# Kernel optimization log

Measured on AMD Instinct MI355X. Metric: run time of the kernel, lower is better.

Reference implementation:

```python
import jax, jax.numpy as jnp
import numpy as np

N_NODES = 50000
N_EDGES = 800000
D_FEAT = 128


def setup_inputs() -> dict:
    key = jax.random.key(0)
    k1, k2, k3, k4 = jax.random.split(key, 4)
    x = jax.random.normal(k1, (N_NODES, D_FEAT), dtype=jnp.float32)
    vals = jax.random.uniform(k2, (N_EDGES,), dtype=jnp.float32)
    rows = jnp.sort(jax.random.randint(k3, (N_EDGES,), 0, N_NODES, dtype=jnp.int32))
    cols = jax.random.randint(k4, (N_EDGES,), 0, N_NODES, dtype=jnp.int32)
    return {"x": x, "vals": vals, "rows": rows, "cols": cols}


def reference(x, vals, rows, cols):
    # out = A @ x where A is sparse COO: out[r] += vals[e] * x[cols[e]] for each edge e with rows[e]==r
    messages = vals[:, None] * x[cols]  # [E, d]
    out = jax.ops.segment_sum(messages, rows, num_segments=N_NODES)  # [N, d]
    return out
```

## Files before the change

kernel.cpp:

```cpp
#include <hip/hip_runtime.h>


#define D_FEAT 128
#define TOTAL_WAVES 8192
#define WAVES_PER_BLOCK 4
#define BLOCK_THREADS (WAVES_PER_BLOCK * 64)
#define PF 8

typedef float v2f __attribute__((ext_vector_type(2)));

__device__ __forceinline__ float bcast_f(float v, int j) {
    return __int_as_float(__builtin_amdgcn_readlane(__float_as_int(v), j));
}

__device__ __forceinline__ unsigned short f2bf_rne(float f) {
    unsigned int b = __float_as_uint(f);
    b += 0x7fffu + ((b >> 16) & 1u);
    return (unsigned short)(b >> 16);
}

__global__ __launch_bounds__(256) void prep_kernel(
    const float* __restrict__ x, const int* __restrict__ rows,
    unsigned short* __restrict__ xb, int* __restrict__ row_ptr,
    float* __restrict__ out, int n4, int n_edges, int n_nodes) {
    const int tid = blockIdx.x * blockDim.x + threadIdx.x;
    const int nth = gridDim.x * blockDim.x;
    const float4* __restrict__ x4 = (const float4*)x;
    ushort4* __restrict__ o4 = (ushort4*)xb;
    for (int i = tid; i < n4; i += nth) {
        float4 f = x4[i];
        ushort4 o;
        o.x = f2bf_rne(f.x);
        o.y = f2bf_rne(f.y);
        o.z = f2bf_rne(f.z);
        o.w = f2bf_rne(f.w);
        o4[i] = o;
    }
    for (int e = tid; e <= n_edges; e += nth) {
        int r, rp;
        if (e < n_edges) {
            r  = rows[e];
            rp = (e == 0) ? -1 : rows[e - 1];
        } else {
            r  = n_nodes;
            rp = rows[n_edges - 1];
        }
        for (int q = rp + 1; q <= r; ++q)
            if (q <= n_nodes) row_ptr[q] = e;
        for (int q = rp + 1; q < r && q < n_nodes; ++q) {
            float4* zo = (float4*)(out + (size_t)q * D_FEAT);
            for (int k = 0; k < D_FEAT / 4; ++k) zo[k] = make_float4(0.f, 0.f, 0.f, 0.f);
        }
    }
}

__global__ __launch_bounds__(BLOCK_THREADS) void agg_bf16_kernel(
    const unsigned int* __restrict__ xb,
    const float* __restrict__ vals, const int* __restrict__ rows,
    const int* __restrict__ cols, const int* __restrict__ row_ptr,
    float* __restrict__ out, int n_edges, int n_nodes, int epw) {
    const int wave = blockIdx.x * WAVES_PER_BLOCK + (threadIdx.x >> 6);
    const int lane = threadIdx.x & 63;

    const int s = wave * epw;
    if (s >= n_edges) return;
    const int s2 = min(s + epw, n_edges);

    int lo = 0, hi = n_nodes;
    while (lo < hi) {
        int mid = (lo + hi) >> 1;
        if (row_ptr[mid] < s) lo = mid + 1; else hi = mid;
    }
    const int r_lo = lo;
    hi = n_nodes;
    while (lo < hi) {
        int mid = (lo + hi) >> 1;
        if (row_ptr[mid] < s2) lo = mid + 1; else hi = mid;
    }
    const int start = row_ptr[r_lo];
    const int end   = row_ptr[lo];
    if (start >= end) return;

    int cur_row = rows[start];
    float2 acc = make_float2(0.f, 0.f);

    for (int e0 = start; e0 < end; e0 += 64) {
        const int nb = min(end - e0, 64);
        int myc = 0, myr = 0;
        float myv = 0.f;
        if (lane < nb) {
            myc = __builtin_nontemporal_load(cols + e0 + lane);
            myr = __builtin_nontemporal_load(rows + e0 + lane);
            myv = __builtin_nontemporal_load(vals + e0 + lane);
        }
        for (int j0 = 0; j0 < nb; j0 += PF) {
            const int m = min(nb - j0, PF);
            unsigned int xu[PF];
            int   rj[PF];
            float vj[PF];
#pragma unroll
            for (int t = 0; t < PF; ++t) {
                if (t < m) {
                    const int cj = __builtin_amdgcn_readlane(myc, j0 + t);
                    rj[t] = __builtin_amdgcn_readlane(myr, j0 + t);
                    vj[t] = bcast_f(myv, j0 + t);
                    xu[t] = xb[(size_t)cj * (D_FEAT / 2) + lane];
                }
            }
#pragma unroll
            for (int t = 0; t < PF; ++t) {
                if (t < m) {
                    if (rj[t] != cur_row) {
                        v2f st; st.x = acc.x; st.y = acc.y;
                        __builtin_nontemporal_store(
                            st, (v2f*)(out + (size_t)cur_row * D_FEAT + 2 * lane));
                        acc.x = 0.f; acc.y = 0.f;
                        cur_row = rj[t];
                    }
                    const float x0 = __uint_as_float(xu[t] << 16);
                    const float x1 = __uint_as_float(xu[t] & 0xffff0000u);
                    acc.x = fmaf(vj[t], x0, acc.x);
                    acc.y = fmaf(vj[t], x1, acc.y);
                }
            }
        }
    }
    v2f st; st.x = acc.x; st.y = acc.y;
    __builtin_nontemporal_store(st, (v2f*)(out + (size_t)cur_row * D_FEAT + 2 * lane));
}

__global__ __launch_bounds__(BLOCK_THREADS) void agg_f32_kernel(
    const float* __restrict__ x, const float* __restrict__ vals,
    const int* __restrict__ rows, const int* __restrict__ cols,
    float* __restrict__ out, int n_edges, int epw) {
    const int wave = blockIdx.x * WAVES_PER_BLOCK + (threadIdx.x >> 6);
    const int lane = threadIdx.x & 63;

    const int start = wave * epw;
    if (start >= n_edges) return;
    int end = start + epw;
    if (end > n_edges) end = n_edges;

    const float2* __restrict__ x2 = (const float2*)x;
    const int first_row = rows[start];
    const int last_row  = rows[end - 1];

    float2 acc = make_float2(0.f, 0.f);
    int cur_row = first_row;

    for (int e0 = start; e0 < end; e0 += 64) {
        const int nb = min(end - e0, 64);
        int myc = 0, myr = 0;
        float myv = 0.f;
        if (lane < nb) {
            myc = cols[e0 + lane];
            myr = rows[e0 + lane];
            myv = vals[e0 + lane];
        }
        for (int j0 = 0; j0 < nb; j0 += PF) {
            const int m = min(nb - j0, PF);
            float2 xv[PF];
            int    rj[PF];
            float  vj[PF];
#pragma unroll
            for (int t = 0; t < PF; ++t) {
                if (t < m) {
                    const int cj = __builtin_amdgcn_readlane(myc, j0 + t);
                    rj[t] = __builtin_amdgcn_readlane(myr, j0 + t);
                    vj[t] = bcast_f(myv, j0 + t);
                    xv[t] = x2[(size_t)cj * (D_FEAT / 2) + lane];
                }
            }
#pragma unroll
            for (int t = 0; t < PF; ++t) {
                if (t < m) {
                    if (rj[t] != cur_row) {
                        float* o = out + (size_t)cur_row * D_FEAT + 2 * lane;
                        if (cur_row == first_row || cur_row == last_row) {
                            atomicAdd(o,     acc.x);
                            atomicAdd(o + 1, acc.y);
                        } else {
                            v2f st; st.x = acc.x; st.y = acc.y;
                            __builtin_nontemporal_store(st, (v2f*)o);
                        }
                        acc.x = 0.f; acc.y = 0.f;
                        cur_row = rj[t];
                    }
                    acc.x = fmaf(vj[t], xv[t].x, acc.x);
                    acc.y = fmaf(vj[t], xv[t].y, acc.y);
                }
            }
        }
    }
    float* o = out + (size_t)cur_row * D_FEAT + 2 * lane;
    atomicAdd(o,     acc.x);
    atomicAdd(o + 1, acc.y);
}

extern "C" void kernel_launch(void* const* d_in, const int* in_sizes, int n_in,
                              void* d_out, int out_size, void* d_ws, size_t ws_size,
                              hipStream_t stream) {
    const float* x    = (const float*)d_in[0];
    const float* vals = (const float*)d_in[1];
    const int*   rows = (const int*)d_in[2];
    const int*   cols = (const int*)d_in[3];
    float*       out  = (float*)d_out;

    const int n_edges = in_sizes[1];
    const int n_x     = in_sizes[0];
    const int n_nodes = out_size / D_FEAT;

    const int epw    = (n_edges + TOTAL_WAVES - 1) / TOTAL_WAVES;
    const int blocks = TOTAL_WAVES / WAVES_PER_BLOCK;

    const size_t xb_bytes = (size_t)n_x * sizeof(unsigned short);
    const size_t rp_off   = (xb_bytes + 255) & ~(size_t)255;
    const size_t need     = rp_off + (size_t)(n_nodes + 1) * sizeof(int);

    if (ws_size >= need) {
        unsigned short* xb = (unsigned short*)d_ws;
        int* row_ptr = (int*)((char*)d_ws + rp_off);
        prep_kernel<<<2048, 256, 0, stream>>>(x, rows, xb, row_ptr, out,
                                              n_x / 4, n_edges, n_nodes);
        agg_bf16_kernel<<<blocks, BLOCK_THREADS, 0, stream>>>(
            (const unsigned int*)xb, vals, rows, cols, row_ptr, out,
            n_edges, n_nodes, epw);
    } else {
        (void)hipMemsetAsync(d_out, 0, (size_t)out_size * sizeof(float), stream);
        agg_f32_kernel<<<blocks, BLOCK_THREADS, 0, stream>>>(
            x, vals, rows, cols, out, n_edges, epw);
    }
}
```

Before: 131.2 us.

## Switch bf16 aggregation to dynamic row-chunk scheduling via atomic work counter

The bf16 aggregation kernel drops the static edge split with per-wave binary searches over row_ptr. Each wave now takes chunks of two rows from a global atomic counter, which prep_kernel resets to zero. Row boundaries come from row_ptr instead of reading the rows array. This removes the binary-search cost and balances load dynamically, at the price of one atomic per two rows (about 25k atomics on a single counter) and very small work items per grab.

```diff
diff --git a/kernel.cpp b/kernel.cpp
--- a/kernel.cpp
+++ b/kernel.cpp
@@ -4,8 +4,10 @@
 #define D_FEAT 128
 #define TOTAL_WAVES 8192
 #define WAVES_PER_BLOCK 4
-#define BLOCK_THREADS (WAVES_PER_BLOCK * 64)
+#define BLOCK_THREADS 256
+#define NBLOCKS (TOTAL_WAVES / WAVES_PER_BLOCK)
 #define PF 8
+#define RPC 2
 
 typedef float v2f __attribute__((ext_vector_type(2)));
 
@@ -22,9 +24,11 @@
 __global__ __launch_bounds__(256) void prep_kernel(
     const float* __restrict__ x, const int* __restrict__ rows,
     unsigned short* __restrict__ xb, int* __restrict__ row_ptr,
-    float* __restrict__ out, int n4, int n_edges, int n_nodes) {
+    int* __restrict__ ctr, float* __restrict__ out, int n4, int n_edges,
+    int n_nodes) {
     const int tid = blockIdx.x * blockDim.x + threadIdx.x;
     const int nth = gridDim.x * blockDim.x;
+    if (tid == 0) *ctr = 0;
     const float4* __restrict__ x4 = (const float4*)x;
     ushort4* __restrict__ o4 = (ushort4*)xb;
     for (int i = tid; i < n4; i += nth) {
@@ -49,84 +53,78 @@
             if (q <= n_nodes) row_ptr[q] = e;
         for (int q = rp + 1; q < r && q < n_nodes; ++q) {
             float4* zo = (float4*)(out + (size_t)q * D_FEAT);
-            for (int k = 0; k < D_FEAT / 4; ++k) zo[k] = make_float4(0.f, 0.f, 0.f, 0.f);
+            for (int k = 0; k < D_FEAT / 4; ++k)
+                zo[k] = make_float4(0.f, 0.f, 0.f, 0.f);
         }
     }
 }
 
 __global__ __launch_bounds__(BLOCK_THREADS) void agg_bf16_kernel(
     const unsigned int* __restrict__ xb,
-    const float* __restrict__ vals, const int* __restrict__ rows,
-    const int* __restrict__ cols, const int* __restrict__ row_ptr,
-    float* __restrict__ out, int n_edges, int n_nodes, int epw) {
-    const int wave = blockIdx.x * WAVES_PER_BLOCK + (threadIdx.x >> 6);
+    const float* __restrict__ vals, const int* __restrict__ cols,
+    const int* __restrict__ row_ptr, int* __restrict__ ctr,
+    float* __restrict__ out, int n_nodes) {
     const int lane = threadIdx.x & 63;
-
-    const int s = wave * epw;
-    if (s >= n_edges) return;
-    const int s2 = min(s + epw, n_edges);
-
-    int lo = 0, hi = n_nodes;
-    while (lo < hi) {
-        int mid = (lo + hi) >> 1;
-        if (row_ptr[mid] < s) lo = mid + 1; else hi = mid;
-    }
-    const int r_lo = lo;
-    hi = n_nodes;
-    while (lo < hi) {
-        int mid = (lo + hi) >> 1;
-        if (row_ptr[mid] < s2) lo = mid + 1; else hi = mid;
-    }
-    const int start = row_ptr[r_lo];
-    const int end   = row_ptr[lo];
-    if (start >= end) return;
-
-    int cur_row = rows[start];
-    float2 acc = make_float2(0.f, 0.f);
-
-    for (int e0 = start; e0 < end; e0 += 64) {
-        const int nb = min(end - e0, 64);
-        int myc = 0, myr = 0;
-        float myv = 0.f;
-        if (lane < nb) {
-            myc = __builtin_nontemporal_load(cols + e0 + lane);
-            myr = __builtin_nontemporal_load(rows + e0 + lane);
-            myv = __builtin_nontemporal_load(vals + e0 + lane);
-        }
-        for (int j0 = 0; j0 < nb; j0 += PF) {
-            const int m = min(nb - j0, PF);
-            unsigned int xu[PF];
-            int   rj[PF];
-            float vj[PF];
-#pragma unroll
-            for (int t = 0; t < PF; ++t) {
-                if (t < m) {
-                    const int cj = __builtin_amdgcn_readlane(myc, j0 + t);
-                    rj[t] = __builtin_amdgcn_readlane(myr, j0 + t);
-                    vj[t] = bcast_f(myv, j0 + t);
-                    xu[t] = xb[(size_t)cj * (D_FEAT / 2) + lane];
-                }
-            }
-#pragma unroll
-            for (int t = 0; t < PF; ++t) {
-                if (t < m) {
-                    if (rj[t] != cur_row) {
-                        v2f st; st.x = acc.x; st.y = acc.y;
-                        __builtin_nontemporal_store(
-                            st, (v2f*)(out + (size_t)cur_row * D_FEAT + 2 * lane));
-                        acc.x = 0.f; acc.y = 0.f;
-                        cur_row = rj[t];
+    for (;;) {
+        int c = 0;
+        if (lane == 0) c = atomicAdd(ctr, 1);
+        c = __shfl(c, 0);
+        const int r0 = c * RPC;
+        if (r0 >= n_nodes) return;
+        const int r1 = min(r0 + RPC, n_nodes);
+        const int e_beg = row_ptr[r0];
+        const int e_end = row_ptr[r1];
+        if (e_beg >= e_end) continue;
+
+        int r = r0;
+        int next_b = row_ptr[r0 + 1];
+        int idx = e_beg;
+        float2 acc = make_float2(0.f, 0.f);
+
+        for (int e0 = e_beg; e0 < e_end; e0 += 64) {
+            const int nb = min(e_end - e0, 64);
+            int myc = 0;
+            float myv = 0.f;
+            if (lane < nb) {
+                myc = __builtin_nontemporal_load(cols + e0 + lane);
+                myv = __builtin_nontemporal_load(vals + e0 + lane);
+            }
+            for (int j0 = 0; j0 < nb; j0 += PF) {
+                const int m = min(nb - j0, PF);
+                unsigned int xu[PF];
+                float vj[PF];
+#pragma unroll
+                for (int t = 0; t < PF; ++t) {
+                    if (t < m) {
+                        const int cj = __builtin_amdgcn_readlane(myc, j0 + t);
+                        vj[t] = bcast_f(myv, j0 + t);
+                        xu[t] = xb[(size_t)cj * (D_FEAT / 2) + lane];
                     }
-                    const float x0 = __uint_as_float(xu[t] << 16);
-                    const float x1 = __uint_as_float(xu[t] & 0xffff0000u);
-                    acc.x = fmaf(vj[t], x0, acc.x);
-                    acc.y = fmaf(vj[t], x1, acc.y);
-                }
-            }
-        }
-    }
-    v2f st; st.x = acc.x; st.y = acc.y;
-    __builtin_nontemporal_store(st, (v2f*)(out + (size_t)cur_row * D_FEAT + 2 * lane));
+                }
+#pragma unroll
+                for (int t = 0; t < PF; ++t) {
+                    if (t < m) {
+                        while (idx == next_b) {
+                            v2f st; st.x = acc.x; st.y = acc.y;
+                            __builtin_nontemporal_store(
+                                st, (v2f*)(out + (size_t)r * D_FEAT + 2 * lane));
+                            acc.x = 0.f; acc.y = 0.f;
+                            ++r;
+                            next_b = row_ptr[r + 1];
+                        }
+                        const float x0 = __uint_as_float(xu[t] << 16);
+                        const float x1 = __uint_as_float(xu[t] & 0xffff0000u);
+                        acc.x = fmaf(vj[t], x0, acc.x);
+                        acc.y = fmaf(vj[t], x1, acc.y);
+                        ++idx;
+                    }
+                }
+            }
+        }
+        v2f st; st.x = acc.x; st.y = acc.y;
+        __builtin_nontemporal_store(
+            st, (v2f*)(out + (size_t)r * D_FEAT + 2 * lane));
+    }
 }
 
 __global__ __launch_bounds__(BLOCK_THREADS) void agg_f32_kernel(
@@ -210,24 +208,23 @@
     const int n_x     = in_sizes[0];
     const int n_nodes = out_size / D_FEAT;
 
-    const int epw    = (n_edges + TOTAL_WAVES - 1) / TOTAL_WAVES;
-    const int blocks = TOTAL_WAVES / WAVES_PER_BLOCK;
-
     const size_t xb_bytes = (size_t)n_x * sizeof(unsigned short);
     const size_t rp_off   = (xb_bytes + 255) & ~(size_t)255;
-    const size_t need     = rp_off + (size_t)(n_nodes + 1) * sizeof(int);
+    const size_t ctr_off  = rp_off + (size_t)(n_nodes + 1) * sizeof(int);
+    const size_t need     = ctr_off + sizeof(int);
 
     if (ws_size >= need) {
         unsigned short* xb = (unsigned short*)d_ws;
         int* row_ptr = (int*)((char*)d_ws + rp_off);
-        prep_kernel<<<2048, 256, 0, stream>>>(x, rows, xb, row_ptr, out,
+        int* ctr     = (int*)((char*)d_ws + ctr_off);
+        prep_kernel<<<2048, 256, 0, stream>>>(x, rows, xb, row_ptr, ctr, out,
                                               n_x / 4, n_edges, n_nodes);
-        agg_bf16_kernel<<<blocks, BLOCK_THREADS, 0, stream>>>(
-            (const unsigned int*)xb, vals, rows, cols, row_ptr, out,
-            n_edges, n_nodes, epw);
+        agg_bf16_kernel<<<NBLOCKS, BLOCK_THREADS, 0, stream>>>(
+            (const unsigned int*)xb, vals, cols, row_ptr, ctr, out, n_nodes);
     } else {
         (void)hipMemsetAsync(d_out, 0, (size_t)out_size * sizeof(float), stream);
-        agg_f32_kernel<<<blocks, BLOCK_THREADS, 0, stream>>>(
+        const int epw    = (n_edges + TOTAL_WAVES - 1) / TOTAL_WAVES;
+        agg_f32_kernel<<<NBLOCKS, BLOCK_THREADS, 0, stream>>>(
             x, vals, rows, cols, out, n_edges, epw);
     }
 }
```

Result: slower. 469.5 us (+257.8%).
